# Optimization experiments

Measured on AMD Instinct MI355X. Metric: run time of the kernel, lower is better.

## Reference

```python
import jax, jax.numpy as jnp
import numpy as np

B, L, D, A, OUT, HID_FC = 4, 4096, 128, 16, 2, 24


def setup_inputs() -> dict:
    key = jax.random.key(0)
    ks = jax.random.split(key, 8)
    xn = lambda k, shape: (jax.random.normal(k, shape, dtype=jnp.float32)
                           * np.sqrt(2.0 / (shape[0] + shape[1])))
    return {
        "x": jax.random.normal(ks[0], (B, L, D), dtype=jnp.float32),
        "fc1_w": xn(ks[1], (D, D)),
        "fc1_b": jnp.zeros((D,), dtype=jnp.float32),
        "Wq_w": xn(ks[2], (D, D)),
        "Wk_w": xn(ks[3], (D, D)),
        "Wv_w": xn(ks[4], (D, D)),
        "fc2_w": xn(ks[5], (D, HID_FC)),
        "fc2_b": jnp.zeros((HID_FC,), dtype=jnp.float32),
        "fc3_w": xn(ks[6], (HID_FC, OUT)),
        "fc3_b": jnp.zeros((OUT,), dtype=jnp.float32),
        "atten_size": A,
        "hidden_size": D,
    }


def _attention(x, Wq_w, Wk_w, Wv_w, atten_size, sqrt_hidden):
    b, l, d = x.shape
    W = 2 * atten_size + 1
    # zero-pad sequence dim, then gather local windows.
    # Faithful to roll-based construction: x_nei[b,i,j] = x[b, i + atten_size - j] (0 if out of range)
    padded = jnp.pad(x, ((0, 0), (atten_size, atten_size), (0, 0)))
    idx = jnp.arange(l)[:, None] + 2 * atten_size - jnp.arange(W)[None, :]  # [L, W]
    x_nei = padded[:, idx]                      # [B, L, W, D]
    q = (x @ Wq_w)[:, :, None, :]               # [B, L, 1, D]
    k = x_nei @ Wk_w                            # [B, L, W, D]
    dsc = jnp.einsum('blod,blwd->blow', q, k) / sqrt_hidden  # [B, L, 1, W]
    # Original torch code: Softmax(dim=2) over the singleton dim -> all-ones (faithful)
    a = jax.nn.softmax(dsc, axis=2)             # [B, L, 1, W]
    v = x_nei @ Wv_w                            # [B, L, W, D]
    out = jnp.squeeze(a @ v, axis=2)            # [B, L, D]
    return out, a


def reference(x, fc1_w, fc1_b, Wq_w, Wk_w, Wv_w, fc2_w, fc2_b, fc3_w, fc3_b,
              atten_size, hidden_size):
    sqrt_hidden = np.sqrt(float(hidden_size))
    h = jax.nn.relu(x @ fc1_w + fc1_b)
    h, a = _attention(h, Wq_w, Wk_w, Wv_w, atten_size, sqrt_hidden)
    h = jax.nn.relu(h @ fc2_w + fc2_b)
    out = h @ fc3_w + fc3_b
    return out, a
```

## Files before the change

kernel.cpp:

```cpp
#include <hip/hip_runtime.h>

constexpr int Bv   = 4;
constexpr int Lv   = 4096;
constexpr int Dv   = 128;
constexpr int Av   = 16;
constexpr int Wwin = 2*Av + 1;
constexpr int OUTv = 2;
constexpr int HIDv = 24;
constexpr int NROWS = Bv * Lv;

constexpr int TILE  = 32;
constexpr int SROWS = TILE + 2*Av;
constexpr int NBLK  = NROWS / TILE;

typedef __attribute__((ext_vector_type(8))) short short8;
typedef __attribute__((ext_vector_type(4))) short short4v;
typedef __attribute__((ext_vector_type(4))) float f32x4;

__device__ __forceinline__ short f2bf(float f) {
    unsigned u = __builtin_bit_cast(unsigned, f);
    u += 0x7FFFu + ((u >> 16) & 1u);
    return (short)(u >> 16);
}

__global__ __launch_bounds__(256) void k_all(const float* __restrict__ x,
                                             const float* __restrict__ W1,
                                             const float* __restrict__ b1,
                                             const float* __restrict__ Wv,
                                             const float* __restrict__ fc2,
                                             const float* __restrict__ fc2b,
                                             const float* __restrict__ fc3w,
                                             const float* __restrict__ fc3b,
                                             float* __restrict__ out,
                                             float* __restrict__ aout) {
    __shared__ short sA[SROWS][136];
    __shared__ short sH[SROWS][136];
    __shared__ short sWfT[32][136];
    __shared__ float smv[SROWS][25];
    __shared__ float sh2[TILE][25];
    __shared__ float sb1[Dv];

    const int t = threadIdx.x, blk = blockIdx.x;
    const int g0 = blk * TILE;
    const int bb = g0 >> 12;
    const int l0 = g0 & (Lv - 1);
    const int lane = t & 63, w = t >> 6;
    const int arow = lane & 15;
    const int kgrp = (lane >> 4) * 8;
    const int crow = (lane >> 4) * 4;
    const int ncol0 = w * 32;

    for (int i = t; i < SROWS*32; i += 256) {
        const int r = i >> 5, c4 = i & 31;
        const int l = l0 - Av + r;
        short4v o = {0, 0, 0, 0};
        if (l >= 0 && l < Lv) {
            const float4 v = *(const float4*)&x[((size_t)bb*Lv + l)*Dv + c4*4];
            o[0] = f2bf(v.x); o[1] = f2bf(v.y); o[2] = f2bf(v.z); o[3] = f2bf(v.w);
        }
        *(short4v*)&sA[r][c4*4] = o;
    }
    if (t < Dv) sb1[t] = b1[t];

    {
        float4* a4 = (float4*)aout;
        const float4 one4 = {1.f, 1.f, 1.f, 1.f};
        for (int i = t; i < 264; i += 256)
            a4[(size_t)blk*264 + i] = one4;
    }

    short8 pb0[4], pb1[4];
    {
        const int n0 = ncol0 + arow, n1 = ncol0 + 16 + arow;
#pragma unroll
        for (int kb = 0; kb < 4; ++kb) {
            const int kof = kb*32 + kgrp;
            float a0[8], a1[8];
#pragma unroll
            for (int j = 0; j < 8; ++j) {
                a0[j] = W1[(size_t)(kof + j)*Dv + n0];
                a1[j] = W1[(size_t)(kof + j)*Dv + n1];
            }
            short8 b0, b1v;
#pragma unroll
            for (int j = 0; j < 8; ++j) { b0[j] = f2bf(a0[j]); b1v[j] = f2bf(a1[j]); }
            pb0[kb] = b0; pb1[kb] = b1v;
        }
    }

    {
        f32x4 accW[2][2];
#pragma unroll
        for (int a = 0; a < 2; ++a) { accW[a][0] = (f32x4){0,0,0,0}; accW[a][1] = (f32x4){0,0,0,0}; }
#pragma unroll
        for (int kb = 0; kb < 4; ++kb) {
            const int kof = kb*32 + kgrp;
            short8 bW[2];
#pragma unroll
            for (int nf = 0; nf < 2; ++nf) {
                const int n = nf*16 + arow;
#pragma unroll
                for (int j = 0; j < 8; ++j) {
                    const float v = (n < HIDv) ? fc2[(size_t)(kof + j)*HIDv + n] : 0.f;
                    bW[nf][j] = f2bf(v);
                }
            }
#pragma unroll
            for (int mf2 = 0; mf2 < 2; ++mf2) {
                const int m = (w*2 + mf2)*16 + arow;
                const float4 v0 = *(const float4*)&Wv[(size_t)m*Dv + kof];
                const float4 v1 = *(const float4*)&Wv[(size_t)m*Dv + kof + 4];
                short8 aW;
                aW[0] = f2bf(v0.x); aW[1] = f2bf(v0.y); aW[2] = f2bf(v0.z); aW[3] = f2bf(v0.w);
                aW[4] = f2bf(v1.x); aW[5] = f2bf(v1.y); aW[6] = f2bf(v1.z); aW[7] = f2bf(v1.w);
                accW[mf2][0] = __builtin_amdgcn_mfma_f32_16x16x32_bf16(aW, bW[0], accW[mf2][0], 0, 0, 0);
                accW[mf2][1] = __builtin_amdgcn_mfma_f32_16x16x32_bf16(aW, bW[1], accW[mf2][1], 0, 0, 0);
            }
        }
#pragma unroll
        for (int mf2 = 0; mf2 < 2; ++mf2) {
#pragma unroll
            for (int nf = 0; nf < 2; ++nf) {
                const int n = nf*16 + arow;
                const int m = (w*2 + mf2)*16 + crow;
                short4v o;
                o[0] = f2bf(accW[mf2][nf][0]);
                o[1] = f2bf(accW[mf2][nf][1]);
                o[2] = f2bf(accW[mf2][nf][2]);
                o[3] = f2bf(accW[mf2][nf][3]);
                *(short4v*)&sWfT[n][m] = o;
            }
        }
    }
    __syncthreads();

    {
        f32x4 acc[4][2];
#pragma unroll
        for (int mf = 0; mf < 4; ++mf) { acc[mf][0] = (f32x4){0,0,0,0}; acc[mf][1] = (f32x4){0,0,0,0}; }

#pragma unroll
        for (int kb = 0; kb < 4; ++kb) {
            const int kof = kb*32 + kgrp;
#pragma unroll
            for (int mf = 0; mf < 4; ++mf) {
                const short8 af = *(const short8*)&sA[mf*16 + arow][kof];
                acc[mf][0] = __builtin_amdgcn_mfma_f32_16x16x32_bf16(af, pb0[kb], acc[mf][0], 0, 0, 0);
                acc[mf][1] = __builtin_amdgcn_mfma_f32_16x16x32_bf16(af, pb1[kb], acc[mf][1], 0, 0, 0);
            }
        }

#pragma unroll
        for (int mf = 0; mf < 4; ++mf) {
#pragma unroll
            for (int nf = 0; nf < 2; ++nf) {
                const int col  = ncol0 + nf*16 + arow;
                const float bias = sb1[col];
#pragma unroll
                for (int r = 0; r < 4; ++r) {
                    float h = acc[mf][nf][r] + bias;
                    h = h > 0.f ? h : 0.f;
                    sH[mf*16 + crow + r][col] = f2bf(h);
                }
            }
        }
    }
    __syncthreads();

    f32x4 acc2[2];
    acc2[0] = (f32x4){0,0,0,0};
    acc2[1] = (f32x4){0,0,0,0};
#pragma unroll
    for (int pp = 0; pp < 2; ++pp) {
        const int p = w*2 + pp, mf = p >> 1, nf = p & 1;
#pragma unroll
        for (int kb = 0; kb < 4; ++kb) {
            const int kof = kb*32 + kgrp;
            const short8 af = *(const short8*)&sH[mf*16 + arow][kof];
            const short8 bf = *(const short8*)&sWfT[nf*16 + arow][kof];
            acc2[pp] = __builtin_amdgcn_mfma_f32_16x16x32_bf16(af, bf, acc2[pp], 0, 0, 0);
        }
    }
#pragma unroll
    for (int pp = 0; pp < 2; ++pp) {
        const int p = w*2 + pp, mf = p >> 1, nf = p & 1;
        const int col = nf*16 + arow;
        if (col < HIDv) {
#pragma unroll
            for (int r = 0; r < 4; ++r) {
                const int row = mf*16 + crow + r;
                const int l = l0 - Av + row;
                smv[row][col] = (l >= 0 && l < Lv) ? acc2[pp][r] : 0.f;
            }
        }
    }
    __syncthreads();

    if (t < 96) {
        const int c = t % 24, rg = t / 24;
        const int rb = rg * 8;
        float s = 0.f;
#pragma unroll
        for (int ww = 0; ww < Wwin; ++ww) s += smv[rb + ww][c];
        const float bias = fc2b[c];
#pragma unroll
        for (int r2 = 0; r2 < 8; ++r2) {
            const int rr = rb + r2;
            const float h = s + bias;
            sh2[rr][c] = h > 0.f ? h : 0.f;
            if (r2 < 7) s += smv[rr + Wwin][c] - smv[rr][c];
        }
    }
    __syncthreads();

    if (t < TILE*OUTv) {
        const int r = t >> 1, oc = t & 1;
        float a = fc3b[oc];
#pragma unroll
        for (int c = 0; c < HIDv; ++c)
            a = fmaf(sh2[r][c], fc3w[c*OUTv + oc], a);
        out[(size_t)(g0 + r)*OUTv + oc] = a;
    }
}

extern "C" void kernel_launch(void* const* d_in, const int* in_sizes, int n_in,
                              void* d_out, int out_size, void* d_ws, size_t ws_size,
                              hipStream_t stream) {
    const float* x     = (const float*)d_in[0];
    const float* fc1_w = (const float*)d_in[1];
    const float* fc1_b = (const float*)d_in[2];
    const float* Wv_w  = (const float*)d_in[5];
    const float* fc2_w = (const float*)d_in[6];
    const float* fc2_b = (const float*)d_in[7];
    const float* fc3_w = (const float*)d_in[8];
    const float* fc3_b = (const float*)d_in[9];

    float* out  = (float*)d_out;
    float* aout = (float*)d_out + NROWS * OUTv;

    k_all<<<dim3(NBLK), dim3(256), 0, stream>>>(x, fc1_w, fc1_b, Wv_w, fc2_w,
                                                fc2_b, fc3_w, fc3_b, out, aout);
}
```

Before: 16.96 us.

## Double block to 512 threads and spread MFMA work across eight waves

```diff
diff --git a/kernel.cpp b/kernel.cpp
--- a/kernel.cpp
+++ b/kernel.cpp
@@ -12,6 +12,7 @@
 constexpr int TILE  = 32;
 constexpr int SROWS = TILE + 2*Av;
 constexpr int NBLK  = NROWS / TILE;
+constexpr int NT    = 512;
 
 typedef __attribute__((ext_vector_type(8))) short short8;
 typedef __attribute__((ext_vector_type(4))) short short4v;
@@ -23,16 +24,16 @@
     return (short)(u >> 16);
 }
 
-__global__ __launch_bounds__(256) void k_all(const float* __restrict__ x,
-                                             const float* __restrict__ W1,
-                                             const float* __restrict__ b1,
-                                             const float* __restrict__ Wv,
-                                             const float* __restrict__ fc2,
-                                             const float* __restrict__ fc2b,
-                                             const float* __restrict__ fc3w,
-                                             const float* __restrict__ fc3b,
-                                             float* __restrict__ out,
-                                             float* __restrict__ aout) {
+__global__ __launch_bounds__(NT) void k_all(const float* __restrict__ x,
+                                            const float* __restrict__ W1,
+                                            const float* __restrict__ b1,
+                                            const float* __restrict__ Wv,
+                                            const float* __restrict__ fc2,
+                                            const float* __restrict__ fc2b,
+                                            const float* __restrict__ fc3w,
+                                            const float* __restrict__ fc3b,
+                                            float* __restrict__ out,
+                                            float* __restrict__ aout) {
     __shared__ short sA[SROWS][136];
     __shared__ short sH[SROWS][136];
     __shared__ short sWfT[32][136];
@@ -48,9 +49,9 @@
     const int arow = lane & 15;
     const int kgrp = (lane >> 4) * 8;
     const int crow = (lane >> 4) * 4;
-    const int ncol0 = w * 32;
-
-    for (int i = t; i < SROWS*32; i += 256) {
+    const int ncol0 = w * 16;
+
+    for (int i = t; i < SROWS*32; i += NT) {
         const int r = i >> 5, c4 = i & 31;
         const int l = l0 - Av + r;
         short4v o = {0, 0, 0, 0};
@@ -62,82 +63,71 @@
     }
     if (t < Dv) sb1[t] = b1[t];
 
-    {
-        float4* a4 = (float4*)aout;
+    if (t < 264) {
         const float4 one4 = {1.f, 1.f, 1.f, 1.f};
-        for (int i = t; i < 264; i += 256)
-            a4[(size_t)blk*264 + i] = one4;
-    }
-
-    short8 pb0[4], pb1[4];
-    {
-        const int n0 = ncol0 + arow, n1 = ncol0 + 16 + arow;
-#pragma unroll
-        for (int kb = 0; kb < 4; ++kb) {
-            const int kof = kb*32 + kgrp;
-            float a0[8], a1[8];
-#pragma unroll
-            for (int j = 0; j < 8; ++j) {
+        ((float4*)aout)[(size_t)blk*264 + t] = one4;
+    }
+
+    short8 pb[4];
+    {
+        const int n0 = ncol0 + arow;
+#pragma unroll
+        for (int kb = 0; kb < 4; ++kb) {
+            const int kof = kb*32 + kgrp;
+            float a0[8];
+#pragma unroll
+            for (int j = 0; j < 8; ++j)
                 a0[j] = W1[(size_t)(kof + j)*Dv + n0];
-                a1[j] = W1[(size_t)(kof + j)*Dv + n1];
-            }
-            short8 b0, b1v;
-#pragma unroll
-            for (int j = 0; j < 8; ++j) { b0[j] = f2bf(a0[j]); b1v[j] = f2bf(a1[j]); }
-            pb0[kb] = b0; pb1[kb] = b1v;
-        }
-    }
-
-    {
-        f32x4 accW[2][2];
-#pragma unroll
-        for (int a = 0; a < 2; ++a) { accW[a][0] = (f32x4){0,0,0,0}; accW[a][1] = (f32x4){0,0,0,0}; }
-#pragma unroll
-        for (int kb = 0; kb < 4; ++kb) {
-            const int kof = kb*32 + kgrp;
-            short8 bW[2];
+            short8 b0;
+#pragma unroll
+            for (int j = 0; j < 8; ++j) b0[j] = f2bf(a0[j]);
+            pb[kb] = b0;
+        }
+    }
+
+    {
+        f32x4 accW[2];
+        accW[0] = (f32x4){0,0,0,0};
+        accW[1] = (f32x4){0,0,0,0};
+#pragma unroll
+        for (int kb = 0; kb < 4; ++kb) {
+            const int kof = kb*32 + kgrp;
+            const int m = w*16 + arow;
+            const float4 v0 = *(const float4*)&Wv[(size_t)m*Dv + kof];
+            const float4 v1 = *(const float4*)&Wv[(size_t)m*Dv + kof + 4];
+            short8 aW;
+            aW[0] = f2bf(v0.x); aW[1] = f2bf(v0.y); aW[2] = f2bf(v0.z); aW[3] = f2bf(v0.w);
+            aW[4] = f2bf(v1.x); aW[5] = f2bf(v1.y); aW[6] = f2bf(v1.z); aW[7] = f2bf(v1.w);
 #pragma unroll
             for (int nf = 0; nf < 2; ++nf) {
                 const int n = nf*16 + arow;
+                short8 bW;
 #pragma unroll
                 for (int j = 0; j < 8; ++j) {
                     const float v = (n < HIDv) ? fc2[(size_t)(kof + j)*HIDv + n] : 0.f;
-                    bW[nf][j] = f2bf(v);
+                    bW[j] = f2bf(v);
                 }
-            }
-#pragma unroll
-            for (int mf2 = 0; mf2 < 2; ++mf2) {
-                const int m = (w*2 + mf2)*16 + arow;
-                const float4 v0 = *(const float4*)&Wv[(size_t)m*Dv + kof];
-                const float4 v1 = *(const float4*)&Wv[(size_t)m*Dv + kof + 4];
-                short8 aW;
-                aW[0] = f2bf(v0.x); aW[1] = f2bf(v0.y); aW[2] = f2bf(v0.z); aW[3] = f2bf(v0.w);
-                aW[4] = f2bf(v1.x); aW[5] = f2bf(v1.y); aW[6] = f2bf(v1.z); aW[7] = f2bf(v1.w);
-                accW[mf2][0] = __builtin_amdgcn_mfma_f32_16x16x32_bf16(aW, bW[0], accW[mf2][0], 0, 0, 0);
-                accW[mf2][1] = __builtin_amdgcn_mfma_f32_16x16x32_bf16(aW, bW[1], accW[mf2][1], 0, 0, 0);
-            }
-        }
-#pragma unroll
-        for (int mf2 = 0; mf2 < 2; ++mf2) {
-#pragma unroll
-            for (int nf = 0; nf < 2; ++nf) {
-                const int n = nf*16 + arow;
-                const int m = (w*2 + mf2)*16 + crow;
-                short4v o;
-                o[0] = f2bf(accW[mf2][nf][0]);
-                o[1] = f2bf(accW[mf2][nf][1]);
-                o[2] = f2bf(accW[mf2][nf][2]);
-                o[3] = f2bf(accW[mf2][nf][3]);
-                *(short4v*)&sWfT[n][m] = o;
-            }
-        }
-    }
-    __syncthreads();
-
-    {
-        f32x4 acc[4][2];
-#pragma unroll
-        for (int mf = 0; mf < 4; ++mf) { acc[mf][0] = (f32x4){0,0,0,0}; acc[mf][1] = (f32x4){0,0,0,0}; }
+                accW[nf] = __builtin_amdgcn_mfma_f32_16x16x32_bf16(aW, bW, accW[nf], 0, 0, 0);
+            }
+        }
+#pragma unroll
+        for (int nf = 0; nf < 2; ++nf) {
+            const int n = nf*16 + arow;
+            const int m = w*16 + crow;
+            short4v o;
+            o[0] = f2bf(accW[nf][0]);
+            o[1] = f2bf(accW[nf][1]);
+            o[2] = f2bf(accW[nf][2]);
+            o[3] = f2bf(accW[nf][3]);
+            *(short4v*)&sWfT[n][m] = o;
+        }
+    }
+    __syncthreads();
+
+    {
+        f32x4 acc[4];
+#pragma unroll
+        for (int mf = 0; mf < 4; ++mf) acc[mf] = (f32x4){0,0,0,0};
 
 #pragma unroll
         for (int kb = 0; kb < 4; ++kb) {
@@ -145,71 +135,53 @@
 #pragma unroll
             for (int mf = 0; mf < 4; ++mf) {
                 const short8 af = *(const short8*)&sA[mf*16 + arow][kof];
-                acc[mf][0] = __builtin_amdgcn_mfma_f32_16x16x32_bf16(af, pb0[kb], acc[mf][0], 0, 0, 0);
-                acc[mf][1] = __builtin_amdgcn_mfma_f32_16x16x32_bf16(af, pb1[kb], acc[mf][1], 0, 0, 0);
-            }
-        }
-
+                acc[mf] = __builtin_amdgcn_mfma_f32_16x16x32_bf16(af, pb[kb], acc[mf], 0, 0, 0);
+            }
+        }
+
+        const int col  = ncol0 + arow;
+        const float bias = sb1[col];
 #pragma unroll
         for (int mf = 0; mf < 4; ++mf) {
 #pragma unroll
-            for (int nf = 0; nf < 2; ++nf) {
-                const int col  = ncol0 + nf*16 + arow;
-                const float bias = sb1[col];
-#pragma unroll
-                for (int r = 0; r < 4; ++r) {
-                    float h = acc[mf][nf][r] + bias;
-                    h = h > 0.f ? h : 0.f;
-                    sH[mf*16 + crow + r][col] = f2bf(h);
-                }
-            }
-        }
-    }
-    __syncthreads();
-
-    f32x4 acc2[2];
-    acc2[0] = (f32x4){0,0,0,0};
-    acc2[1] = (f32x4){0,0,0,0};
-#pragma unroll
-    for (int pp = 0; pp < 2; ++pp) {
-        const int p = w*2 + pp, mf = p >> 1, nf = p & 1;
+            for (int r = 0; r < 4; ++r) {
+                float h = acc[mf][r] + bias;
+                h = h > 0.f ? h : 0.f;
+                sH[mf*16 + crow + r][col] = f2bf(h);
+            }
+        }
+    }
+    __syncthreads();
+
+    {
+        const int mf = w >> 1, nf = w & 1;
+        f32x4 acc2 = (f32x4){0,0,0,0};
 #pragma unroll
         for (int kb = 0; kb < 4; ++kb) {
             const int kof = kb*32 + kgrp;
             const short8 af = *(const short8*)&sH[mf*16 + arow][kof];
             const short8 bf = *(const short8*)&sWfT[nf*16 + arow][kof];
-            acc2[pp] = __builtin_amdgcn_mfma_f32_16x16x32_bf16(af, bf, acc2[pp], 0, 0, 0);
-        }
-    }
-#pragma unroll
-    for (int pp = 0; pp < 2; ++pp) {
-        const int p = w*2 + pp, mf = p >> 1, nf = p & 1;
+            acc2 = __builtin_amdgcn_mfma_f32_16x16x32_bf16(af, bf, acc2, 0, 0, 0);
+        }
         const int col = nf*16 + arow;
         if (col < HIDv) {
 #pragma unroll
             for (int r = 0; r < 4; ++r) {
                 const int row = mf*16 + crow + r;
                 const int l = l0 - Av + row;
-                smv[row][col] = (l >= 0 && l < Lv) ? acc2[pp][r] : 0.f;
-            }
-        }
-    }
-    __syncthreads();
-
-    if (t < 96) {
-        const int c = t % 24, rg = t / 24;
-        const int rb = rg * 8;
+                smv[row][col] = (l >= 0 && l < Lv) ? acc2[r] : 0.f;
+            }
+        }
+    }
+    __syncthreads();
+
+    for (int i = t; i < TILE*HIDv; i += NT) {
+        const int r = i / HIDv, c = i % HIDv;
         float s = 0.f;
 #pragma unroll
-        for (int ww = 0; ww < Wwin; ++ww) s += smv[rb + ww][c];
-        const float bias = fc2b[c];
-#pragma unroll
-        for (int r2 = 0; r2 < 8; ++r2) {
-            const int rr = rb + r2;
-            const float h = s + bias;
-            sh2[rr][c] = h > 0.f ? h : 0.f;
-            if (r2 < 7) s += smv[rr + Wwin][c] - smv[rr][c];
-        }
+        for (int ww = 0; ww < Wwin; ++ww) s += smv[r + ww][c];
+        const float h = s + fc2b[c];
+        sh2[r][c] = h > 0.f ? h : 0.f;
     }
     __syncthreads();
 
@@ -238,6 +210,6 @@
     float* out  = (float*)d_out;
     float* aout = (float*)d_out + NROWS * OUTv;
 
-    k_all<<<dim3(NBLK), dim3(256), 0, stream>>>(x, fc1_w, fc1_b, Wv_w, fc2_w,
-                                                fc2_b, fc3_w, fc3_b, out, aout);
+    k_all<<<dim3(NBLK), dim3(NT), 0, stream>>>(x, fc1_w, fc1_b, Wv_w, fc2_w,
+                                               fc2_b, fc3_w, fc3_b, out, aout);
 }
```

After: 17.64 us. 1.04x slower.
